# Optimization experiments

Hardware: AMD Instinct MI355X
Metric: run time of the kernel (lower is better)

The kernel has to match this reference:

```python
import jax, jax.numpy as jnp
import numpy as np
import math

D_MODEL, N_HEADS, D_K, D_V = 512, 2, 64, 64
C_CLIP = 10.0
MASK_FILL = -10.0

def setup_inputs() -> dict:
    key = jax.random.key(0)
    ks = jax.random.split(key, 12)
    B, Lq, Lk = 4, 2048, 2048
    s = 1.0 / math.sqrt(D_MODEL)
    return {
        "Q": jax.random.normal(ks[0], (B, Lq, D_MODEL), jnp.float32),
        "K": jax.random.normal(ks[1], (B, Lk, D_MODEL), jnp.float32),
        "V": jax.random.normal(ks[2], (B, Lk, D_MODEL), jnp.float32),
        "mask": jax.random.randint(ks[3], (B, Lk), 0, 2) > 0,
        "Wq": jax.random.normal(ks[4], (D_MODEL, N_HEADS * D_K), jnp.float32) * s,
        "bq": jnp.zeros((N_HEADS * D_K,), jnp.float32),
        "Wk": jax.random.normal(ks[5], (D_MODEL, N_HEADS * D_K), jnp.float32) * s,
        "bk": jnp.zeros((N_HEADS * D_K,), jnp.float32),
        "Wv": jax.random.normal(ks[6], (D_MODEL, N_HEADS * D_V), jnp.float32) * s,
        "bv": jnp.zeros((N_HEADS * D_V,), jnp.float32),
        "Wo": jax.random.normal(ks[7], (N_HEADS * D_V, D_MODEL), jnp.float32) * s,
        "bo": jnp.zeros((D_MODEL,), jnp.float32),
    }

def reference(Q, K, V, mask, Wq, bq, Wk, bk, Wv, bv, Wo, bo):
    B, Lq, _ = Q.shape
    Lk = K.shape[1]
    # project and split heads: [B, h, L, d]
    q = (Q @ Wq + bq).reshape(B, Lq, N_HEADS, D_K).transpose(0, 2, 1, 3)
    k = (K @ Wk + bk).reshape(B, Lk, N_HEADS, D_K).transpose(0, 2, 1, 3)
    v = (V @ Wv + bv).reshape(B, Lk, N_HEADS, D_V).transpose(0, 2, 1, 3)
    scores = jnp.einsum("bhqd,bhkd->bhqk", q, k) / jnp.sqrt(jnp.float32(D_K))
    scores = jnp.tanh(scores) * C_CLIP
    scores = jnp.where(mask[:, None, None, :], MASK_FILL, scores)
    attn = jax.nn.log_softmax(scores, axis=-1)  # NOTE: log-softmax used directly as weights
    out = jnp.einsum("bhqk,bhkd->bhqd", attn, v)
    out = out.transpose(0, 2, 1, 3).reshape(B, Lq, N_HEADS * D_V)
    out = out @ Wo + bo
    return (out, attn)
```

## Files before the change

kernel.cpp:

```cpp
#include <hip/hip_runtime.h>

typedef __attribute__((ext_vector_type(8))) short short8;
typedef __attribute__((ext_vector_type(4))) short short4v;
typedef __attribute__((ext_vector_type(4))) float f32x4;

#define DEVI static __device__ __forceinline__

constexpr int NB   = 4;
constexpr int NH   = 2;
constexpr int SEQ  = 2048;
constexpr int DM   = 512;
constexpr int DKV  = 64;
constexpr int HDIM = 128;

DEVI unsigned short f2bf(float f) {
    union { float f; unsigned u; } v; v.f = f;
    unsigned r = v.u + 0x7FFFu + ((v.u >> 16) & 1u);
    return (unsigned short)(r >> 16);
}
DEVI float bf2f(unsigned short s) {
    union { unsigned u; float f; } v; v.u = ((unsigned)s) << 16; return v.f;
}
DEVI void async16(const void* g, void* l) {
    __builtin_amdgcn_global_load_lds(
        (const __attribute__((address_space(1))) unsigned int*)g,
        (__attribute__((address_space(3))) unsigned int*)l, 16, 0, 0);
}

__global__ __launch_bounds__(256) void k_prep(
    const float* __restrict__ Wq, const float* __restrict__ Wk,
    const float* __restrict__ Wv, const float* __restrict__ Wo,
    unsigned short* __restrict__ Wqt, unsigned short* __restrict__ Wkt,
    unsigned short* __restrict__ Wvt, unsigned short* __restrict__ Wot) {
    int id = blockIdx.x * 256 + threadIdx.x;
    int which = id >> 16;
    int rem = id & 65535;
    if (which < 3) {
        const float* W = which == 0 ? Wq : (which == 1 ? Wk : Wv);
        unsigned short* Wt = which == 0 ? Wqt : (which == 1 ? Wkt : Wvt);
        int n = rem >> 9, k = rem & 511;
        Wt[rem] = f2bf(W[k * HDIM + n]);
    } else {
        int n = rem >> 7, k = rem & 127;
        Wot[rem] = f2bf(Wo[k * DM + n]);
    }
}

__global__ __launch_bounds__(256) void k_proj(
    const float* __restrict__ Qg, const float* __restrict__ Kg, const float* __restrict__ Vg,
    const unsigned short* __restrict__ Wqt, const unsigned short* __restrict__ Wkt,
    const unsigned short* __restrict__ Wvt,
    const float* __restrict__ bq, const float* __restrict__ bk, const float* __restrict__ bv,
    unsigned short* __restrict__ qs, unsigned short* __restrict__ kb,
    unsigned short* __restrict__ vt) {
    __shared__ unsigned short lA[64 * 64];
    __shared__ unsigned short lB[128 * 64];

    const int y = blockIdx.y;
    const float* X = y == 0 ? Qg : (y == 1 ? Kg : Vg);
    const unsigned short* Wt = y == 0 ? Wqt : (y == 1 ? Wkt : Wvt);
    const float* bias = y == 0 ? bq : (y == 1 ? bk : bv);
    const float scal = y == 0 ? 0.125f : 1.0f;
    const int row0 = blockIdx.x * 64;
    const int tid = threadIdx.x, lane = tid & 63, wv = tid >> 6;
    const int l16 = lane & 15, lq4 = lane >> 4;
    const int wr = wv >> 1, wc = wv & 1;

    f32x4 acc[2][4];
    #pragma unroll
    for (int i = 0; i < 2; ++i)
        #pragma unroll
        for (int j = 0; j < 4; ++j) acc[i][j] = f32x4{0.f, 0.f, 0.f, 0.f};

    const int arow = tid >> 2, ac0 = (tid & 3) * 16;

    for (int kc = 0; kc < 8; ++kc) {
        {
            const float* src = X + (size_t)(row0 + arow) * DM + kc * 64 + ac0;
            unsigned short* dst = &lA[arow * 64 + ac0];
            #pragma unroll
            for (int i = 0; i < 4; ++i) {
                float4 v = *(const float4*)(src + 4 * i);
                unsigned p0 = (unsigned)f2bf(v.x) | ((unsigned)f2bf(v.y) << 16);
                unsigned p1 = (unsigned)f2bf(v.z) | ((unsigned)f2bf(v.w) << 16);
                *(unsigned*)(dst + 4 * i) = p0;
                *(unsigned*)(dst + 4 * i + 2) = p1;
            }
        }
        #pragma unroll
        for (int c = 0; c < 4; ++c) {
            int chunk = wv * 4 + c;
            int n = chunk * 8 + (lane >> 3);
            int kpart = (lane & 7) * 8;
            const void* g = (const char*)Wt + ((size_t)n * DM + kc * 64 + kpart) * 2;
            void* l = (char*)lB + chunk * 1024 + lane * 16;
            async16(g, l);
        }
        __syncthreads();

        #pragma unroll
        for (int ks = 0; ks < 2; ++ks) {
            short8 a[2], b[4];
            #pragma unroll
            for (int mt = 0; mt < 2; ++mt) {
                int m = wr * 32 + mt * 16 + l16;
                a[mt] = *(const short8*)&lA[m * 64 + ks * 32 + lq4 * 8];
            }
            #pragma unroll
            for (int nt = 0; nt < 4; ++nt) {
                int n = wc * 64 + nt * 16 + l16;
                b[nt] = *(const short8*)&lB[n * 64 + ks * 32 + lq4 * 8];
            }
            #pragma unroll
            for (int mt = 0; mt < 2; ++mt)
                #pragma unroll
                for (int nt = 0; nt < 4; ++nt)
                    acc[mt][nt] = __builtin_amdgcn_mfma_f32_16x16x32_bf16(
                        a[mt], b[nt], acc[mt][nt], 0, 0, 0);
        }
        __syncthreads();
    }

    if (y < 2) {
        unsigned short* dstp = (y == 0) ? qs : kb;
        #pragma unroll
        for (int mt = 0; mt < 2; ++mt)
            #pragma unroll
            for (int nt = 0; nt < 4; ++nt) {
                int col = wc * 64 + nt * 16 + l16;
                float bb = bias[col];
                int h = col >> 6, d = col & 63;
                #pragma unroll
                for (int r = 0; r < 4; ++r) {
                    int row = row0 + wr * 32 + mt * 16 + lq4 * 4 + r;
                    int b = row >> 11, pos = row & 2047;
                    float val = (acc[mt][nt][r] + bb) * scal;
                    dstp[((size_t)(b * NH + h) * SEQ + pos) * DKV + d] = f2bf(val);
                }
            }
    } else {
        #pragma unroll
        for (int mt = 0; mt < 2; ++mt)
            #pragma unroll
            for (int nt = 0; nt < 4; ++nt) {
                int col = wc * 64 + nt * 16 + l16;
                float bb = bias[col];
                #pragma unroll
                for (int r = 0; r < 4; ++r) {
                    int mrow = wr * 32 + mt * 16 + lq4 * 4 + r;
                    lB[col * 64 + mrow] = f2bf(acc[mt][nt][r] + bb);
                }
            }
        __syncthreads();
        int c = tid >> 1, mp = (tid & 1) * 32;
        int b = row0 >> 11, kpos0 = row0 & 2047;
        int h = c >> 6, d = c & 63;
        unsigned short* dst = vt + ((size_t)(b * NH + h) * DKV + d) * SEQ + kpos0 + mp;
        const unsigned short* srcl = &lB[c * 64 + mp];
        #pragma unroll
        for (int i = 0; i < 4; ++i)
            *(uint4*)(dst + 8 * i) = *(const uint4*)(srcl + 8 * i);
    }
}

__global__ __launch_bounds__(256) void k_pass1(
    const unsigned short* __restrict__ qs, const unsigned short* __restrict__ kb,
    const int* __restrict__ maskg, float* __restrict__ Lpart) {
    __shared__ unsigned short lK[128 * 64];
    __shared__ int lM[128];
    __shared__ float lsumW[4 * 64];

    const int bx = blockIdx.x;
    const int ksp = bx & 3;
    const int qt = (bx >> 2) & 31;
    const int bh = bx >> 7;
    const int qbase = qt * 64;
    const int b = bh >> 1;
    const int tid = threadIdx.x, lane = tid & 63, wv = tid >> 6;
    const int l16 = lane & 15, lq4 = lane >> 4;

    short8 aq[4][2];
    #pragma unroll
    for (int mt = 0; mt < 4; ++mt)
        #pragma unroll
        for (int ks = 0; ks < 2; ++ks) {
            size_t off = ((size_t)bh * SEQ + qbase + mt * 16 + l16) * DKV + ks * 32 + lq4 * 8;
            aq[mt][ks] = *(const short8*)(qs + off);
        }

    float sums[4][4];
    #pragma unroll
    for (int mt = 0; mt < 4; ++mt)
        #pragma unroll
        for (int r = 0; r < 4; ++r) sums[mt][r] = 0.f;

    const char* kbase_ptr = (const char*)(kb + (size_t)bh * SEQ * DKV);

    for (int kt = ksp * 4; kt < ksp * 4 + 4; ++kt) {
        int kbase = kt * 128;
        #pragma unroll
        for (int c = 0; c < 4; ++c) {
            int chunk = wv * 4 + c;
            const void* g = kbase_ptr + (size_t)kbase * 128 + chunk * 1024 + lane * 16;
            void* l = (char*)lK + chunk * 1024 + lane * 16;
            async16(g, l);
        }
        if (tid < 128) lM[tid] = maskg[b * SEQ + kbase + tid];
        __syncthreads();

        f32x4 acc[4][2];
        #pragma unroll
        for (int mt = 0; mt < 4; ++mt)
            #pragma unroll
            for (int nt = 0; nt < 2; ++nt) acc[mt][nt] = f32x4{0.f, 0.f, 0.f, 0.f};
        #pragma unroll
        for (int ks = 0; ks < 2; ++ks) {
            short8 bfr[2];
            #pragma unroll
            for (int nt = 0; nt < 2; ++nt) {
                int n = wv * 32 + nt * 16 + l16;
                bfr[nt] = *(const short8*)&lK[n * 64 + ks * 32 + lq4 * 8];
            }
            #pragma unroll
            for (int mt = 0; mt < 4; ++mt)
                #pragma unroll
                for (int nt = 0; nt < 2; ++nt)
                    acc[mt][nt] = __builtin_amdgcn_mfma_f32_16x16x32_bf16(
                        aq[mt][ks], bfr[nt], acc[mt][nt], 0, 0, 0);
        }
        #pragma unroll
        for (int nt = 0; nt < 2; ++nt) {
            int col = wv * 32 + nt * 16 + l16;
            int mv = lM[col];
            #pragma unroll
            for (int mt = 0; mt < 4; ++mt)
                #pragma unroll
                for (int r = 0; r < 4; ++r) {
                    float x = acc[mt][nt][r];
                    float e2 = __expf(2.f * x);
                    float s10 = 10.f - 20.f * __builtin_amdgcn_rcpf(1.f + e2);
                    float s = mv ? -10.f : s10;
                    sums[mt][r] += __expf(s);
                }
        }
        __syncthreads();
    }

    #pragma unroll
    for (int mt = 0; mt < 4; ++mt)
        #pragma unroll
        for (int r = 0; r < 4; ++r) {
            float v = sums[mt][r];
            v += __shfl_xor(v, 1); v += __shfl_xor(v, 2);
            v += __shfl_xor(v, 4); v += __shfl_xor(v, 8);
            if (l16 == 0) lsumW[wv * 64 + mt * 16 + lq4 * 4 + r] = v;
        }
    __syncthreads();
    if (tid < 64) {
        float v = lsumW[tid] + lsumW[64 + tid] + lsumW[128 + tid] + lsumW[192 + tid];
        Lpart[(size_t)ksp * (8 * SEQ) + (size_t)bh * SEQ + qbase + tid] = v;
    }
}

__global__ __launch_bounds__(256) void k_pass2(
    const unsigned short* __restrict__ qs, const unsigned short* __restrict__ kb,
    const unsigned short* __restrict__ vt, const int* __restrict__ maskg,
    const float* __restrict__ Lpart, float* __restrict__ attnG, float* __restrict__ outh2) {
    __shared__ unsigned short lK[128 * 64];
    __shared__ unsigned short lV[64 * 128];
    __shared__ unsigned short lAttn[64 * 136];
    __shared__ int lM[128];

    const int bx = blockIdx.x;
    const int ksp = bx & 3;
    const int qt = (bx >> 2) & 31;
    const int bh = bx >> 7;
    const int qbase = qt * 64;
    const int b = bh >> 1, h = bh & 1;
    const int tid = threadIdx.x, lane = tid & 63, wv = tid >> 6;
    const int l16 = lane & 15, lq4 = lane >> 4;

    short8 aq[4][2];
    #pragma unroll
    for (int mt = 0; mt < 4; ++mt)
        #pragma unroll
        for (int ks = 0; ks < 2; ++ks) {
            size_t off = ((size_t)bh * SEQ + qbase + mt * 16 + l16) * DKV + ks * 32 + lq4 * 8;
            aq[mt][ks] = *(const short8*)(qs + off);
        }

    float Lr[4][4];
    #pragma unroll
    for (int mt = 0; mt < 4; ++mt)
        #pragma unroll
        for (int r = 0; r < 4; ++r) {
            size_t idx = (size_t)bh * SEQ + qbase + mt * 16 + lq4 * 4 + r;
            float s = Lpart[idx] + Lpart[8 * SEQ + idx] +
                      Lpart[2 * 8 * SEQ + idx] + Lpart[3 * 8 * SEQ + idx];
            Lr[mt][r] = __logf(s);
        }

    f32x4 o[4];
    #pragma unroll
    for (int mt = 0; mt < 4; ++mt) o[mt] = f32x4{0.f, 0.f, 0.f, 0.f};

    const char* kbase_ptr = (const char*)(kb + (size_t)bh * SEQ * DKV);

    for (int kt = ksp * 4; kt < ksp * 4 + 4; ++kt) {
        int kbase = kt * 128;
        #pragma unroll
        for (int c = 0; c < 4; ++c) {
            int chunk = wv * 4 + c;
            const void* g = kbase_ptr + (size_t)kbase * 128 + chunk * 1024 + lane * 16;
            void* l = (char*)lK + chunk * 1024 + lane * 16;
            async16(g, l);
        }
        #pragma unroll
        for (int c = 0; c < 4; ++c) {
            int chunk = wv * 4 + c;
            int d = chunk * 4 + (lane >> 4);
            int kk = (lane & 15) * 8;
            const void* g = (const char*)vt + (((size_t)bh * DKV + d) * SEQ + kbase + kk) * 2;
            void* l = (char*)lV + chunk * 1024 + lane * 16;
            async16(g, l);
        }
        if (tid < 128) lM[tid] = maskg[b * SEQ + kbase + tid];
        __syncthreads();

        f32x4 s[4][2];
        #pragma unroll
        for (int mt = 0; mt < 4; ++mt)
            #pragma unroll
            for (int nt = 0; nt < 2; ++nt) s[mt][nt] = f32x4{0.f, 0.f, 0.f, 0.f};
        #pragma unroll
        for (int ks = 0; ks < 2; ++ks) {
            short8 bfr[2];
            #pragma unroll
            for (int nt = 0; nt < 2; ++nt) {
                int n = wv * 32 + nt * 16 + l16;
                bfr[nt] = *(const short8*)&lK[n * 64 + ks * 32 + lq4 * 8];
            }
            #pragma unroll
            for (int mt = 0; mt < 4; ++mt)
                #pragma unroll
                for (int nt = 0; nt < 2; ++nt)
                    s[mt][nt] = __builtin_amdgcn_mfma_f32_16x16x32_bf16(
                        aq[mt][ks], bfr[nt], s[mt][nt], 0, 0, 0);
        }
        #pragma unroll
        for (int nt = 0; nt < 2; ++nt) {
            int col = wv * 32 + nt * 16 + l16;
            int mv = lM[col];
            #pragma unroll
            for (int mt = 0; mt < 4; ++mt)
                #pragma unroll
                for (int r = 0; r < 4; ++r) {
                    float x = s[mt][nt][r];
                    float e2 = __expf(2.f * x);
                    float s10 = 10.f - 20.f * __builtin_amdgcn_rcpf(1.f + e2);
                    float a = (mv ? -10.f : s10) - Lr[mt][r];
                    lAttn[(mt * 16 + lq4 * 4 + r) * 136 + col] = f2bf(a);
                }
        }
        __syncthreads();

        #pragma unroll
        for (int ks = 0; ks < 4; ++ks) {
            short8 bfr = *(const short8*)&lV[(wv * 16 + l16) * 128 + ks * 32 + lq4 * 8];
            #pragma unroll
            for (int mt = 0; mt < 4; ++mt) {
                short8 af = *(const short8*)&lAttn[(mt * 16 + l16) * 136 + ks * 32 + lq4 * 8];
                o[mt] = __builtin_amdgcn_mfma_f32_16x16x32_bf16(af, bfr, o[mt], 0, 0, 0);
            }
        }
        #pragma unroll
        for (int j = 0; j < 8; ++j) {
            int row = j * 8 + (tid >> 5);
            int col = (tid & 31) * 4;
            short4v hv = *(const short4v*)&lAttn[row * 136 + col];
            float4 f;
            f.x = bf2f((unsigned short)hv[0]); f.y = bf2f((unsigned short)hv[1]);
            f.z = bf2f((unsigned short)hv[2]); f.w = bf2f((unsigned short)hv[3]);
            float* gdst = attnG + ((size_t)bh * SEQ + qbase + row) * SEQ + kbase + col;
            *(float4*)gdst = f;
        }
        __syncthreads();
    }

    float* dst = outh2 + (size_t)ksp * (8192 * HDIM);
    #pragma unroll
    for (int mt = 0; mt < 4; ++mt)
        #pragma unroll
        for (int r = 0; r < 4; ++r) {
            int q = qbase + mt * 16 + lq4 * 4 + r;
            int dcol = wv * 16 + l16;
            dst[((size_t)b * SEQ + q) * HDIM + h * DKV + dcol] = o[mt][r];
        }
}

__global__ __launch_bounds__(256) void k_comb(const float* __restrict__ outh2,
                                              unsigned short* __restrict__ outh) {
    int i = (blockIdx.x * 256 + threadIdx.x) * 4;
    float4 a = *(const float4*)(outh2 + i);
    float4 c = *(const float4*)(outh2 + 1048576 + i);
    float4 d = *(const float4*)(outh2 + 2 * 1048576 + i);
    float4 e = *(const float4*)(outh2 + 3 * 1048576 + i);
    unsigned long long pk =
        (unsigned long long)f2bf(a.x + c.x + d.x + e.x) |
        ((unsigned long long)f2bf(a.y + c.y + d.y + e.y) << 16) |
        ((unsigned long long)f2bf(a.z + c.z + d.z + e.z) << 32) |
        ((unsigned long long)f2bf(a.w + c.w + d.w + e.w) << 48);
    *(unsigned long long*)(outh + i) = pk;
}

__global__ __launch_bounds__(256) void k_oproj(
    const unsigned short* __restrict__ outh, const unsigned short* __restrict__ Wot,
    const float* __restrict__ bo, float* __restrict__ outG) {
    __shared__ unsigned short lA2[128 * 128];
    __shared__ unsigned short lB2[128 * 128];
    const int row0 = blockIdx.x * 128, col0 = blockIdx.y * 128;
    const int tid = threadIdx.x, lane = tid & 63, wv = tid >> 6;
    const int l16 = lane & 15, lq4 = lane >> 4;
    const int wr = wv >> 1, wc = wv & 1;

    #pragma unroll
    for (int c = 0; c < 8; ++c) {
        int chunk = wv * 8 + c;
        const void* g = (const char*)outh + (size_t)row0 * 256 + chunk * 1024 + lane * 16;
        void* l = (char*)lA2 + chunk * 1024 + lane * 16;
        async16(g, l);
    }
    #pragma unroll
    for (int c = 0; c < 8; ++c) {
        int chunk = wv * 8 + c;
        const void* g = (const char*)Wot + (size_t)col0 * 256 + chunk * 1024 + lane * 16;
        void* l = (char*)lB2 + chunk * 1024 + lane * 16;
        async16(g, l);
    }
    __syncthreads();

    f32x4 acc[4][4];
    #pragma unroll
    for (int mt = 0; mt < 4; ++mt)
        #pragma unroll
        for (int nt = 0; nt < 4; ++nt) acc[mt][nt] = f32x4{0.f, 0.f, 0.f, 0.f};

    #pragma unroll
    for (int ks = 0; ks < 4; ++ks) {
        short8 a[4], bfr[4];
        #pragma unroll
        for (int mt = 0; mt < 4; ++mt)
            a[mt] = *(const short8*)&lA2[(wr * 64 + mt * 16 + l16) * 128 + ks * 32 + lq4 * 8];
        #pragma unroll
        for (int nt = 0; nt < 4; ++nt)
            bfr[nt] = *(const short8*)&lB2[(wc * 64 + nt * 16 + l16) * 128 + ks * 32 + lq4 * 8];
        #pragma unroll
        for (int mt = 0; mt < 4; ++mt)
            #pragma unroll
            for (int nt = 0; nt < 4; ++nt)
                acc[mt][nt] = __builtin_amdgcn_mfma_f32_16x16x32_bf16(
                    a[mt], bfr[nt], acc[mt][nt], 0, 0, 0);
    }

    #pragma unroll
    for (int nt = 0; nt < 4; ++nt) {
        int col = col0 + wc * 64 + nt * 16 + l16;
        float bb = bo[col];
        #pragma unroll
        for (int mt = 0; mt < 4; ++mt)
            #pragma unroll
            for (int r = 0; r < 4; ++r) {
                int row = row0 + wr * 64 + mt * 16 + lq4 * 4 + r;
                outG[(size_t)row * DM + col] = acc[mt][nt][r] + bb;
            }
    }
}

extern "C" void kernel_launch(void* const* d_in, const int* in_sizes, int n_in,
                              void* d_out, int out_size, void* d_ws, size_t ws_size,
                              hipStream_t stream) {
    (void)in_sizes; (void)n_in; (void)out_size; (void)ws_size;
    const float* Qg = (const float*)d_in[0];
    const float* Kg = (const float*)d_in[1];
    const float* Vg = (const float*)d_in[2];
    const int*   maskg = (const int*)d_in[3];
    const float* Wq = (const float*)d_in[4];
    const float* bq = (const float*)d_in[5];
    const float* Wk = (const float*)d_in[6];
    const float* bk = (const float*)d_in[7];
    const float* Wv = (const float*)d_in[8];
    const float* bv = (const float*)d_in[9];
    const float* Wo = (const float*)d_in[10];
    const float* bo = (const float*)d_in[11];

    char* ws = (char*)d_ws;
    unsigned short* qs   = (unsigned short*)(ws);
    unsigned short* kb   = (unsigned short*)(ws + (4  << 20));
    unsigned short* vt   = (unsigned short*)(ws + (8  << 20));
    float*          outh2= (float*)(ws + (12 << 20));
    unsigned short* outh = (unsigned short*)(ws + (28 << 20));
    float*          Lpart= (float*)(ws + (30 << 20));
    unsigned short* Wqt  = (unsigned short*)(ws + (30 << 20) + 262144);
    unsigned short* Wkt  = (unsigned short*)((char*)Wqt + 131072);
    unsigned short* Wvt  = (unsigned short*)((char*)Wkt + 131072);
    unsigned short* Wot  = (unsigned short*)((char*)Wvt + 131072);

    float* outG  = (float*)d_out;
    float* attnG = outG + (size_t)NB * SEQ * DM;

    hipLaunchKernelGGL(k_prep, dim3(1024), dim3(256), 0, stream,
                       Wq, Wk, Wv, Wo, Wqt, Wkt, Wvt, Wot);
    hipLaunchKernelGGL(k_proj, dim3(128, 3), dim3(256), 0, stream,
                       Qg, Kg, Vg, Wqt, Wkt, Wvt, bq, bk, bv, qs, kb, vt);
    hipLaunchKernelGGL(k_pass1, dim3(1024), dim3(256), 0, stream, qs, kb, maskg, Lpart);
    hipLaunchKernelGGL(k_pass2, dim3(1024), dim3(256), 0, stream,
                       qs, kb, vt, maskg, Lpart, attnG, outh2);
    hipLaunchKernelGGL(k_comb, dim3(1024), dim3(256), 0, stream, outh2, outh);
    hipLaunchKernelGGL(k_oproj, dim3(64, 4), dim3(256), 0, stream, outh, Wot, bo, outG);
}
```

Before: 262.9 us.

## Fuse attention passes into one kernel holding full score rows in LDS

Replaces the two-pass attention (sum pass, recompute-and-write pass) and the split-K combine kernel with one kernel. Each 512-thread block holds a 32-query by 2048-key bf16 score tile in 128KB of LDS, computes the log-sum-exp from it, writes the fp32 attention weights, then runs the PV matmul straight from LDS. This removes the recomputation of QK^T, the partial-sum buffers and the extra launch. It also adds XOR swizzling to the LDS tiles in the projection and output-projection kernels to reduce bank conflicts. The tradeoffs are one block per CU from the large LDS footprint and K/V fragments read straight from global memory without staging.

Result: slower. 281.8 us (+7.2%).

```diff
diff --git a/kernel.cpp b/kernel.cpp
--- a/kernel.cpp
+++ b/kernel.cpp
@@ -1,7 +1,6 @@
 #include <hip/hip_runtime.h>
 
 typedef __attribute__((ext_vector_type(8))) short short8;
-typedef __attribute__((ext_vector_type(4))) short short4v;
 typedef __attribute__((ext_vector_type(4))) float f32x4;
 
 #define DEVI static __device__ __forceinline__
@@ -77,22 +76,23 @@
     for (int kc = 0; kc < 8; ++kc) {
         {
             const float* src = X + (size_t)(row0 + arow) * DM + kc * 64 + ac0;
-            unsigned short* dst = &lA[arow * 64 + ac0];
             #pragma unroll
             for (int i = 0; i < 4; ++i) {
                 float4 v = *(const float4*)(src + 4 * i);
                 unsigned p0 = (unsigned)f2bf(v.x) | ((unsigned)f2bf(v.y) << 16);
                 unsigned p1 = (unsigned)f2bf(v.z) | ((unsigned)f2bf(v.w) << 16);
-                *(unsigned*)(dst + 4 * i) = p0;
-                *(unsigned*)(dst + 4 * i + 2) = p1;
+                int slot = ((tid & 3) * 2 + (i >> 1)) ^ (arow & 7);
+                char* d = (char*)lA + arow * 128 + slot * 16 + (i & 1) * 8;
+                *(unsigned*)d = p0;
+                *(unsigned*)(d + 4) = p1;
             }
         }
         #pragma unroll
         for (int c = 0; c < 4; ++c) {
             int chunk = wv * 4 + c;
             int n = chunk * 8 + (lane >> 3);
-            int kpart = (lane & 7) * 8;
-            const void* g = (const char*)Wt + ((size_t)n * DM + kc * 64 + kpart) * 2;
+            int gslot = (lane & 7) ^ (n & 7);
+            const void* g = (const char*)Wt + ((size_t)n * DM + kc * 64) * 2 + gslot * 16;
             void* l = (char*)lB + chunk * 1024 + lane * 16;
             async16(g, l);
         }
@@ -104,12 +104,14 @@
             #pragma unroll
             for (int mt = 0; mt < 2; ++mt) {
                 int m = wr * 32 + mt * 16 + l16;
-                a[mt] = *(const short8*)&lA[m * 64 + ks * 32 + lq4 * 8];
+                unsigned ao = (unsigned)(m * 128 + ks * 64 + lq4 * 16) ^ ((unsigned)(m & 7) << 4);
+                a[mt] = *(const short8*)((const char*)lA + ao);
             }
             #pragma unroll
             for (int nt = 0; nt < 4; ++nt) {
                 int n = wc * 64 + nt * 16 + l16;
-                b[nt] = *(const short8*)&lB[n * 64 + ks * 32 + lq4 * 8];
+                unsigned bo2 = (unsigned)(n * 128 + ks * 64 + lq4 * 16) ^ ((unsigned)(n & 7) << 4);
+                b[nt] = *(const short8*)((const char*)lB + bo2);
             }
             #pragma unroll
             for (int mt = 0; mt < 2; ++mt)
@@ -163,254 +165,119 @@
     }
 }
 
-__global__ __launch_bounds__(256) void k_pass1(
-    const unsigned short* __restrict__ qs, const unsigned short* __restrict__ kb,
-    const int* __restrict__ maskg, float* __restrict__ Lpart) {
-    __shared__ unsigned short lK[128 * 64];
-    __shared__ int lM[128];
-    __shared__ float lsumW[4 * 64];
-
-    const int bx = blockIdx.x;
-    const int ksp = bx & 3;
-    const int qt = (bx >> 2) & 31;
-    const int bh = bx >> 7;
-    const int qbase = qt * 64;
-    const int b = bh >> 1;
-    const int tid = threadIdx.x, lane = tid & 63, wv = tid >> 6;
-    const int l16 = lane & 15, lq4 = lane >> 4;
-
-    short8 aq[4][2];
-    #pragma unroll
-    for (int mt = 0; mt < 4; ++mt)
-        #pragma unroll
-        for (int ks = 0; ks < 2; ++ks) {
-            size_t off = ((size_t)bh * SEQ + qbase + mt * 16 + l16) * DKV + ks * 32 + lq4 * 8;
-            aq[mt][ks] = *(const short8*)(qs + off);
-        }
-
-    float sums[4][4];
-    #pragma unroll
-    for (int mt = 0; mt < 4; ++mt)
-        #pragma unroll
-        for (int r = 0; r < 4; ++r) sums[mt][r] = 0.f;
-
-    const char* kbase_ptr = (const char*)(kb + (size_t)bh * SEQ * DKV);
-
-    for (int kt = ksp * 4; kt < ksp * 4 + 4; ++kt) {
-        int kbase = kt * 128;
-        #pragma unroll
-        for (int c = 0; c < 4; ++c) {
-            int chunk = wv * 4 + c;
-            const void* g = kbase_ptr + (size_t)kbase * 128 + chunk * 1024 + lane * 16;
-            void* l = (char*)lK + chunk * 1024 + lane * 16;
-            async16(g, l);
-        }
-        if (tid < 128) lM[tid] = maskg[b * SEQ + kbase + tid];
-        __syncthreads();
-
-        f32x4 acc[4][2];
-        #pragma unroll
-        for (int mt = 0; mt < 4; ++mt)
-            #pragma unroll
-            for (int nt = 0; nt < 2; ++nt) acc[mt][nt] = f32x4{0.f, 0.f, 0.f, 0.f};
-        #pragma unroll
-        for (int ks = 0; ks < 2; ++ks) {
-            short8 bfr[2];
-            #pragma unroll
-            for (int nt = 0; nt < 2; ++nt) {
-                int n = wv * 32 + nt * 16 + l16;
-                bfr[nt] = *(const short8*)&lK[n * 64 + ks * 32 + lq4 * 8];
-            }
-            #pragma unroll
-            for (int mt = 0; mt < 4; ++mt)
-                #pragma unroll
-                for (int nt = 0; nt < 2; ++nt)
-                    acc[mt][nt] = __builtin_amdgcn_mfma_f32_16x16x32_bf16(
-                        aq[mt][ks], bfr[nt], acc[mt][nt], 0, 0, 0);
-        }
-        #pragma unroll
-        for (int nt = 0; nt < 2; ++nt) {
-            int col = wv * 32 + nt * 16 + l16;
-            int mv = lM[col];
-            #pragma unroll
-            for (int mt = 0; mt < 4; ++mt)
-                #pragma unroll
-                for (int r = 0; r < 4; ++r) {
-                    float x = acc[mt][nt][r];
-                    float e2 = __expf(2.f * x);
-                    float s10 = 10.f - 20.f * __builtin_amdgcn_rcpf(1.f + e2);
-                    float s = mv ? -10.f : s10;
-                    sums[mt][r] += __expf(s);
-                }
-        }
-        __syncthreads();
-    }
-
-    #pragma unroll
-    for (int mt = 0; mt < 4; ++mt)
-        #pragma unroll
-        for (int r = 0; r < 4; ++r) {
-            float v = sums[mt][r];
-            v += __shfl_xor(v, 1); v += __shfl_xor(v, 2);
-            v += __shfl_xor(v, 4); v += __shfl_xor(v, 8);
-            if (l16 == 0) lsumW[wv * 64 + mt * 16 + lq4 * 4 + r] = v;
-        }
-    __syncthreads();
-    if (tid < 64) {
-        float v = lsumW[tid] + lsumW[64 + tid] + lsumW[128 + tid] + lsumW[192 + tid];
-        Lpart[(size_t)ksp * (8 * SEQ) + (size_t)bh * SEQ + qbase + tid] = v;
-    }
-}
-
-__global__ __launch_bounds__(256) void k_pass2(
+__global__ __launch_bounds__(512) void k_fused(
     const unsigned short* __restrict__ qs, const unsigned short* __restrict__ kb,
     const unsigned short* __restrict__ vt, const int* __restrict__ maskg,
-    const float* __restrict__ Lpart, float* __restrict__ attnG, float* __restrict__ outh2) {
-    __shared__ unsigned short lK[128 * 64];
-    __shared__ unsigned short lV[64 * 128];
-    __shared__ unsigned short lAttn[64 * 136];
-    __shared__ int lM[128];
-
-    const int bx = blockIdx.x;
-    const int ksp = bx & 3;
-    const int qt = (bx >> 2) & 31;
-    const int bh = bx >> 7;
-    const int qbase = qt * 64;
+    float* __restrict__ attnG, unsigned short* __restrict__ outh) {
+    __shared__ unsigned short sAttn[32 * 2048];
+    __shared__ float lsum[4][32];
+    __shared__ float lL[32];
+
+    const int wg = blockIdx.x;
+    const int swz = (wg & 7) * 64 + (wg >> 3);
+    const int bh = swz >> 6;
+    const int qt = swz & 63;
+    const int qbase = qt * 32;
     const int b = bh >> 1, h = bh & 1;
     const int tid = threadIdx.x, lane = tid & 63, wv = tid >> 6;
     const int l16 = lane & 15, lq4 = lane >> 4;
-
-    short8 aq[4][2];
-    #pragma unroll
-    for (int mt = 0; mt < 4; ++mt)
-        #pragma unroll
-        for (int ks = 0; ks < 2; ++ks) {
-            size_t off = ((size_t)bh * SEQ + qbase + mt * 16 + l16) * DKV + ks * 32 + lq4 * 8;
-            aq[mt][ks] = *(const short8*)(qs + off);
-        }
-
-    float Lr[4][4];
-    #pragma unroll
-    for (int mt = 0; mt < 4; ++mt)
+    const int wr = wv >> 2, wc = wv & 3;
+
+    const unsigned short* qrow =
+        qs + ((size_t)bh * SEQ + qbase + wr * 16 + l16) * DKV + lq4 * 8;
+    short8 aq0 = *(const short8*)qrow;
+    short8 aq1 = *(const short8*)(qrow + 32);
+
+    const unsigned short* kfrag =
+        kb + ((size_t)bh * SEQ + wc * 16 + l16) * DKV + lq4 * 8;
+    const int* mrow = maskg + b * SEQ + wc * 16 + l16;
+
+    const int srow_q = wr * 16 + lq4 * 4;
+    const int cbase = wc * 16 + l16;
+
+    float sums[4] = {0.f, 0.f, 0.f, 0.f};
+
+    #pragma unroll 2
+    for (int kt = 0; kt < 32; ++kt) {
+        short8 b0 = *(const short8*)(kfrag + (size_t)kt * 4096);
+        short8 b1 = *(const short8*)(kfrag + (size_t)kt * 4096 + 32);
+        int mv = mrow[kt * 64];
+        f32x4 acc = f32x4{0.f, 0.f, 0.f, 0.f};
+        acc = __builtin_amdgcn_mfma_f32_16x16x32_bf16(aq0, b0, acc, 0, 0, 0);
+        acc = __builtin_amdgcn_mfma_f32_16x16x32_bf16(aq1, b1, acc, 0, 0, 0);
+        int col = kt * 64 + cbase;
         #pragma unroll
         for (int r = 0; r < 4; ++r) {
-            size_t idx = (size_t)bh * SEQ + qbase + mt * 16 + lq4 * 4 + r;
-            float s = Lpart[idx] + Lpart[8 * SEQ + idx] +
-                      Lpart[2 * 8 * SEQ + idx] + Lpart[3 * 8 * SEQ + idx];
-            Lr[mt][r] = __logf(s);
-        }
-
-    f32x4 o[4];
-    #pragma unroll
-    for (int mt = 0; mt < 4; ++mt) o[mt] = f32x4{0.f, 0.f, 0.f, 0.f};
-
-    const char* kbase_ptr = (const char*)(kb + (size_t)bh * SEQ * DKV);
-
-    for (int kt = ksp * 4; kt < ksp * 4 + 4; ++kt) {
-        int kbase = kt * 128;
-        #pragma unroll
-        for (int c = 0; c < 4; ++c) {
-            int chunk = wv * 4 + c;
-            const void* g = kbase_ptr + (size_t)kbase * 128 + chunk * 1024 + lane * 16;
-            void* l = (char*)lK + chunk * 1024 + lane * 16;
-            async16(g, l);
-        }
-        #pragma unroll
-        for (int c = 0; c < 4; ++c) {
-            int chunk = wv * 4 + c;
-            int d = chunk * 4 + (lane >> 4);
-            int kk = (lane & 15) * 8;
-            const void* g = (const char*)vt + (((size_t)bh * DKV + d) * SEQ + kbase + kk) * 2;
-            void* l = (char*)lV + chunk * 1024 + lane * 16;
-            async16(g, l);
-        }
-        if (tid < 128) lM[tid] = maskg[b * SEQ + kbase + tid];
-        __syncthreads();
-
-        f32x4 s[4][2];
-        #pragma unroll
-        for (int mt = 0; mt < 4; ++mt)
-            #pragma unroll
-            for (int nt = 0; nt < 2; ++nt) s[mt][nt] = f32x4{0.f, 0.f, 0.f, 0.f};
-        #pragma unroll
-        for (int ks = 0; ks < 2; ++ks) {
-            short8 bfr[2];
-            #pragma unroll
-            for (int nt = 0; nt < 2; ++nt) {
-                int n = wv * 32 + nt * 16 + l16;
-                bfr[nt] = *(const short8*)&lK[n * 64 + ks * 32 + lq4 * 8];
-            }
-            #pragma unroll
-            for (int mt = 0; mt < 4; ++mt)
-                #pragma unroll
-                for (int nt = 0; nt < 2; ++nt)
-                    s[mt][nt] = __builtin_amdgcn_mfma_f32_16x16x32_bf16(
-                        aq[mt][ks], bfr[nt], s[mt][nt], 0, 0, 0);
-        }
-        #pragma unroll
-        for (int nt = 0; nt < 2; ++nt) {
-            int col = wv * 32 + nt * 16 + l16;
-            int mv = lM[col];
-            #pragma unroll
-            for (int mt = 0; mt < 4; ++mt)
-                #pragma unroll
-                for (int r = 0; r < 4; ++r) {
-                    float x = s[mt][nt][r];
-                    float e2 = __expf(2.f * x);
-                    float s10 = 10.f - 20.f * __builtin_amdgcn_rcpf(1.f + e2);
-                    float a = (mv ? -10.f : s10) - Lr[mt][r];
-                    lAttn[(mt * 16 + lq4 * 4 + r) * 136 + col] = f2bf(a);
-                }
-        }
-        __syncthreads();
-
-        #pragma unroll
-        for (int ks = 0; ks < 4; ++ks) {
-            short8 bfr = *(const short8*)&lV[(wv * 16 + l16) * 128 + ks * 32 + lq4 * 8];
-            #pragma unroll
-            for (int mt = 0; mt < 4; ++mt) {
-                short8 af = *(const short8*)&lAttn[(mt * 16 + l16) * 136 + ks * 32 + lq4 * 8];
-                o[mt] = __builtin_amdgcn_mfma_f32_16x16x32_bf16(af, bfr, o[mt], 0, 0, 0);
-            }
-        }
-        #pragma unroll
-        for (int j = 0; j < 8; ++j) {
-            int row = j * 8 + (tid >> 5);
-            int col = (tid & 31) * 4;
-            short4v hv = *(const short4v*)&lAttn[row * 136 + col];
-            float4 f;
-            f.x = bf2f((unsigned short)hv[0]); f.y = bf2f((unsigned short)hv[1]);
-            f.z = bf2f((unsigned short)hv[2]); f.w = bf2f((unsigned short)hv[3]);
-            float* gdst = attnG + ((size_t)bh * SEQ + qbase + row) * SEQ + kbase + col;
-            *(float4*)gdst = f;
-        }
-        __syncthreads();
-    }
-
-    float* dst = outh2 + (size_t)ksp * (8192 * HDIM);
-    #pragma unroll
-    for (int mt = 0; mt < 4; ++mt)
-        #pragma unroll
-        for (int r = 0; r < 4; ++r) {
-            int q = qbase + mt * 16 + lq4 * 4 + r;
-            int dcol = wv * 16 + l16;
-            dst[((size_t)b * SEQ + q) * HDIM + h * DKV + dcol] = o[mt][r];
-        }
-}
-
-__global__ __launch_bounds__(256) void k_comb(const float* __restrict__ outh2,
-                                              unsigned short* __restrict__ outh) {
-    int i = (blockIdx.x * 256 + threadIdx.x) * 4;
-    float4 a = *(const float4*)(outh2 + i);
-    float4 c = *(const float4*)(outh2 + 1048576 + i);
-    float4 d = *(const float4*)(outh2 + 2 * 1048576 + i);
-    float4 e = *(const float4*)(outh2 + 3 * 1048576 + i);
-    unsigned long long pk =
-        (unsigned long long)f2bf(a.x + c.x + d.x + e.x) |
-        ((unsigned long long)f2bf(a.y + c.y + d.y + e.y) << 16) |
-        ((unsigned long long)f2bf(a.z + c.z + d.z + e.z) << 32) |
-        ((unsigned long long)f2bf(a.w + c.w + d.w + e.w) << 48);
-    *(unsigned long long*)(outh + i) = pk;
+            float x = acc[r];
+            float e2 = __expf(2.f * x);
+            float s10 = 10.f - 20.f * __builtin_amdgcn_rcpf(1.f + e2);
+            float s = mv ? -10.f : s10;
+            sums[r] += __expf(s);
+            int row = srow_q + r;
+            unsigned bo = (unsigned)(row * 4096 + col * 2) ^ ((unsigned)(row & 7) << 4);
+            *(unsigned short*)((char*)sAttn + bo) = f2bf(s);
+        }
+    }
+
+    #pragma unroll
+    for (int r = 0; r < 4; ++r) {
+        float v = sums[r];
+        v += __shfl_xor(v, 1); v += __shfl_xor(v, 2);
+        v += __shfl_xor(v, 4); v += __shfl_xor(v, 8);
+        if (l16 == 0) lsum[wc][srow_q + r] = v;
+    }
+    __syncthreads();
+    if (tid < 32)
+        lL[tid] = __logf(lsum[0][tid] + lsum[1][tid] + lsum[2][tid] + lsum[3][tid]);
+    __syncthreads();
+
+    {
+        const int row = tid >> 4;
+        const int cb = (tid & 15) * 8;
+        const float Lv = lL[row];
+        float* gdst = attnG + ((size_t)bh * SEQ + qbase + row) * SEQ;
+        const unsigned rbase = (unsigned)(row * 4096);
+        const unsigned rxor = (unsigned)(row & 7) << 4;
+        #pragma unroll
+        for (int j = 0; j < 16; ++j) {
+            int c = cb + j * 128;
+            unsigned bo = (rbase + (unsigned)(c * 2)) ^ rxor;
+            short8 v = *(const short8*)((const char*)sAttn + bo);
+            float fv[8];
+            #pragma unroll
+            for (int t = 0; t < 8; ++t) fv[t] = bf2f((unsigned short)v[t]) - Lv;
+            float4 fa, fb;
+            fa.x = fv[0]; fa.y = fv[1]; fa.z = fv[2]; fa.w = fv[3];
+            fb.x = fv[4]; fb.y = fv[5]; fb.z = fv[6]; fb.w = fv[7];
+            *(float4*)(gdst + c) = fa;
+            *(float4*)(gdst + c + 4) = fb;
+            short8 w;
+            #pragma unroll
+            for (int t = 0; t < 8; ++t) w[t] = (short)f2bf(fv[t]);
+            *(short8*)((char*)sAttn + bo) = w;
+        }
+    }
+    __syncthreads();
+
+    const unsigned short* vfrag =
+        vt + ((size_t)bh * DKV + wc * 16 + l16) * SEQ + lq4 * 8;
+    const int arow = wr * 16 + l16;
+    const unsigned abase = (unsigned)(arow * 4096);
+    const unsigned axor = (unsigned)(arow & 7) << 4;
+    f32x4 o = f32x4{0.f, 0.f, 0.f, 0.f};
+    #pragma unroll 4
+    for (int ks = 0; ks < 64; ++ks) {
+        short8 af = *(const short8*)((const char*)sAttn +
+                                     ((abase + (unsigned)(ks * 64 + lq4 * 16)) ^ axor));
+        short8 vf = *(const short8*)(vfrag + ks * 32);
+        o = __builtin_amdgcn_mfma_f32_16x16x32_bf16(af, vf, o, 0, 0, 0);
+    }
+
+    #pragma unroll
+    for (int r = 0; r < 4; ++r) {
+        size_t orow = (size_t)b * SEQ + qbase + wr * 16 + lq4 * 4 + r;
+        outh[orow * HDIM + h * DKV + wc * 16 + l16] = f2bf(o[r]);
+    }
 }
 
 __global__ __launch_bounds__(256) void k_oproj(
@@ -426,16 +293,18 @@
     #pragma unroll
     for (int c = 0; c < 8; ++c) {
         int chunk = wv * 8 + c;
-        const void* g = (const char*)outh + (size_t)row0 * 256 + chunk * 1024 + lane * 16;
-        void* l = (char*)lA2 + chunk * 1024 + lane * 16;
-        async16(g, l);
+        int row = chunk * 4 + (lane >> 4);
+        int gslot = (lane & 15) ^ (row & 7);
+        async16((const char*)outh + ((size_t)(row0 + row)) * 256 + gslot * 16,
+                (char*)lA2 + chunk * 1024 + lane * 16);
     }
     #pragma unroll
     for (int c = 0; c < 8; ++c) {
         int chunk = wv * 8 + c;
-        const void* g = (const char*)Wot + (size_t)col0 * 256 + chunk * 1024 + lane * 16;
-        void* l = (char*)lB2 + chunk * 1024 + lane * 16;
-        async16(g, l);
+        int row = chunk * 4 + (lane >> 4);
+        int gslot = (lane & 15) ^ (row & 7);
+        async16((const char*)Wot + ((size_t)(col0 + row)) * 256 + gslot * 16,
+                (char*)lB2 + chunk * 1024 + lane * 16);
     }
     __syncthreads();
 
@@ -449,11 +318,17 @@
     for (int ks = 0; ks < 4; ++ks) {
         short8 a[4], bfr[4];
         #pragma unroll
-        for (int mt = 0; mt < 4; ++mt)
-            a[mt] = *(const short8*)&lA2[(wr * 64 + mt * 16 + l16) * 128 + ks * 32 + lq4 * 8];
-        #pragma unroll
-        for (int nt = 0; nt < 4; ++nt)
-            bfr[nt] = *(const short8*)&lB2[(wc * 64 + nt * 16 + l16) * 128 + ks * 32 + lq4 * 8];
+        for (int mt = 0; mt < 4; ++mt) {
+            int m = wr * 64 + mt * 16 + l16;
+            unsigned ao = (unsigned)(m * 256 + ks * 64 + lq4 * 16) ^ ((unsigned)(m & 7) << 4);
+            a[mt] = *(const short8*)((const char*)lA2 + ao);
+        }
+        #pragma unroll
+        for (int nt = 0; nt < 4; ++nt) {
+            int n = wc * 64 + nt * 16 + l16;
+            unsigned bo2 = (unsigned)(n * 256 + ks * 64 + lq4 * 16) ^ ((unsigned)(n & 7) << 4);
+            bfr[nt] = *(const short8*)((const char*)lB2 + bo2);
+        }
         #pragma unroll
         for (int mt = 0; mt < 4; ++mt)
             #pragma unroll
@@ -497,9 +372,7 @@
     unsigned short* qs   = (unsigned short*)(ws);
     unsigned short* kb   = (unsigned short*)(ws + (4  << 20));
     unsigned short* vt   = (unsigned short*)(ws + (8  << 20));
-    float*          outh2= (float*)(ws + (12 << 20));
     unsigned short* outh = (unsigned short*)(ws + (28 << 20));
-    float*          Lpart= (float*)(ws + (30 << 20));
     unsigned short* Wqt  = (unsigned short*)(ws + (30 << 20) + 262144);
     unsigned short* Wkt  = (unsigned short*)((char*)Wqt + 131072);
     unsigned short* Wvt  = (unsigned short*)((char*)Wkt + 131072);
@@ -512,9 +385,7 @@
                        Wq, Wk, Wv, Wo, Wqt, Wkt, Wvt, Wot);
     hipLaunchKernelGGL(k_proj, dim3(128, 3), dim3(256), 0, stream,
                        Qg, Kg, Vg, Wqt, Wkt, Wvt, bq, bk, bv, qs, kb, vt);
-    hipLaunchKernelGGL(k_pass1, dim3(1024), dim3(256), 0, stream, qs, kb, maskg, Lpart);
-    hipLaunchKernelGGL(k_pass2, dim3(1024), dim3(256), 0, stream,
-                       qs, kb, vt, maskg, Lpart, attnG, outh2);
-    hipLaunchKernelGGL(k_comb, dim3(1024), dim3(256), 0, stream, outh2, outh);
+    hipLaunchKernelGGL(k_fused, dim3(512), dim3(512), 0, stream,
+                       qs, kb, vt, maskg, attnG, outh);
     hipLaunchKernelGGL(k_oproj, dim3(64, 4), dim3(256), 0, stream, outh, Wot, bo, outG);
 }
```

## Fuse split-K combine into output projection, tile weight transpose, swizzle LDS

Applied to the files above, without the earlier changes.

Removes the separate k_comb kernel. The output-projection kernel now reads the four fp32 split partials directly, sums them, converts to bf16 and writes them into LDS. The weight-prep kernel now does a tiled transpose through shared memory with vectorized loads and stores, replacing strided scalar accesses. An XOR swizzle is applied to LDS rows in k_oproj to cut bank conflicts. The trade-off is that each of the 4 column blocks of k_oproj re-reads and re-sums the same partials, so fp32 partial traffic is multiplied by four.

New measurement: 259.3 us. About the same (-1.4%).

```diff
diff --git a/kernel.cpp b/kernel.cpp
--- a/kernel.cpp
+++ b/kernel.cpp
@@ -21,6 +21,9 @@
 DEVI float bf2f(unsigned short s) {
     union { unsigned u; float f; } v; v.u = ((unsigned)s) << 16; return v.f;
 }
+DEVI unsigned pk2(float a, float b) {
+    return (unsigned)f2bf(a) | ((unsigned)f2bf(b) << 16);
+}
 DEVI void async16(const void* g, void* l) {
     __builtin_amdgcn_global_load_lds(
         (const __attribute__((address_space(1))) unsigned int*)g,
@@ -32,18 +35,37 @@
     const float* __restrict__ Wv, const float* __restrict__ Wo,
     unsigned short* __restrict__ Wqt, unsigned short* __restrict__ Wkt,
     unsigned short* __restrict__ Wvt, unsigned short* __restrict__ Wot) {
-    int id = blockIdx.x * 256 + threadIdx.x;
-    int which = id >> 16;
-    int rem = id & 65535;
-    if (which < 3) {
-        const float* W = which == 0 ? Wq : (which == 1 ? Wk : Wv);
-        unsigned short* Wt = which == 0 ? Wqt : (which == 1 ? Wkt : Wvt);
-        int n = rem >> 9, k = rem & 511;
-        Wt[rem] = f2bf(W[k * HDIM + n]);
+    __shared__ unsigned short T[64][72];
+    const int bid = blockIdx.x, tid = threadIdx.x;
+    const float* src; unsigned short* dst; int ss, ds, k0, n0;
+    if (bid < 48) {
+        int m = bid >> 4, t16 = bid & 15;
+        src = m == 0 ? Wq : (m == 1 ? Wk : Wv);
+        dst = m == 0 ? Wqt : (m == 1 ? Wkt : Wvt);
+        ss = 128; ds = 512;
+        k0 = (t16 >> 1) * 64; n0 = (t16 & 1) * 64;
     } else {
-        int n = rem >> 7, k = rem & 127;
-        Wot[rem] = f2bf(Wo[k * DM + n]);
-    }
+        int t16 = bid - 48;
+        src = Wo; dst = Wot; ss = 512; ds = 128;
+        k0 = (t16 >> 3) * 64; n0 = (t16 & 7) * 64;
+    }
+    const int kk = tid >> 4, nn4 = (tid & 15) * 4;
+    #pragma unroll
+    for (int i = 0; i < 4; ++i) {
+        float4 v = *(const float4*)(src + (size_t)(k0 + kk + i * 16) * ss + n0 + nn4);
+        T[kk + i * 16][nn4]     = f2bf(v.x);
+        T[kk + i * 16][nn4 + 1] = f2bf(v.y);
+        T[kk + i * 16][nn4 + 2] = f2bf(v.z);
+        T[kk + i * 16][nn4 + 3] = f2bf(v.w);
+    }
+    __syncthreads();
+    const int nn = tid >> 2, kc = (tid & 3) * 16;
+    unsigned short tmp[16];
+    #pragma unroll
+    for (int i = 0; i < 16; ++i) tmp[i] = T[kc + i][nn];
+    unsigned short* o = dst + (size_t)(n0 + nn) * ds + k0 + kc;
+    *(uint4*)o       = *(uint4*)tmp;
+    *(uint4*)(o + 8) = *(uint4*)(tmp + 8);
 }
 
 __global__ __launch_bounds__(256) void k_proj(
@@ -398,23 +420,8 @@
         }
 }
 
-__global__ __launch_bounds__(256) void k_comb(const float* __restrict__ outh2,
-                                              unsigned short* __restrict__ outh) {
-    int i = (blockIdx.x * 256 + threadIdx.x) * 4;
-    float4 a = *(const float4*)(outh2 + i);
-    float4 c = *(const float4*)(outh2 + 1048576 + i);
-    float4 d = *(const float4*)(outh2 + 2 * 1048576 + i);
-    float4 e = *(const float4*)(outh2 + 3 * 1048576 + i);
-    unsigned long long pk =
-        (unsigned long long)f2bf(a.x + c.x + d.x + e.x) |
-        ((unsigned long long)f2bf(a.y + c.y + d.y + e.y) << 16) |
-        ((unsigned long long)f2bf(a.z + c.z + d.z + e.z) << 32) |
-        ((unsigned long long)f2bf(a.w + c.w + d.w + e.w) << 48);
-    *(unsigned long long*)(outh + i) = pk;
-}
-
 __global__ __launch_bounds__(256) void k_oproj(
-    const unsigned short* __restrict__ outh, const unsigned short* __restrict__ Wot,
+    const float* __restrict__ outh2, const unsigned short* __restrict__ Wot,
     const float* __restrict__ bo, float* __restrict__ outG) {
     __shared__ unsigned short lA2[128 * 128];
     __shared__ unsigned short lB2[128 * 128];
@@ -426,16 +433,29 @@
     #pragma unroll
     for (int c = 0; c < 8; ++c) {
         int chunk = wv * 8 + c;
-        const void* g = (const char*)outh + (size_t)row0 * 256 + chunk * 1024 + lane * 16;
-        void* l = (char*)lA2 + chunk * 1024 + lane * 16;
-        async16(g, l);
-    }
-    #pragma unroll
-    for (int c = 0; c < 8; ++c) {
-        int chunk = wv * 8 + c;
-        const void* g = (const char*)Wot + (size_t)col0 * 256 + chunk * 1024 + lane * 16;
-        void* l = (char*)lB2 + chunk * 1024 + lane * 16;
-        async16(g, l);
+        int row = chunk * 4 + (lane >> 4);
+        int gslot = (lane & 15) ^ (row & 7);
+        async16((const char*)Wot + ((size_t)(col0 + row)) * 256 + gslot * 16,
+                (char*)lB2 + chunk * 1024 + lane * 16);
+    }
+    {
+        const int c16 = tid & 31;
+        const int rb = tid >> 5;
+        #pragma unroll
+        for (int i = 0; i < 16; ++i) {
+            int r = rb + i * 8;
+            size_t off = (size_t)(row0 + r) * 128 + c16 * 4;
+            float4 a = *(const float4*)(outh2 + off);
+            float4 b = *(const float4*)(outh2 + 1048576 + off);
+            float4 c = *(const float4*)(outh2 + 2 * 1048576 + off);
+            float4 d = *(const float4*)(outh2 + 3 * 1048576 + off);
+            unsigned p0 = pk2(a.x + b.x + c.x + d.x, a.y + b.y + c.y + d.y);
+            unsigned p1 = pk2(a.z + b.z + c.z + d.z, a.w + b.w + c.w + d.w);
+            unsigned long long pk =
+                (unsigned long long)p0 | ((unsigned long long)p1 << 32);
+            unsigned bo2 = (unsigned)(r * 256 + c16 * 8) ^ ((unsigned)(r & 7) << 4);
+            *(unsigned long long*)((char*)lA2 + bo2) = pk;
+        }
     }
     __syncthreads();
 
@@ -449,11 +469,17 @@
     for (int ks = 0; ks < 4; ++ks) {
         short8 a[4], bfr[4];
         #pragma unroll
-        for (int mt = 0; mt < 4; ++mt)
-            a[mt] = *(const short8*)&lA2[(wr * 64 + mt * 16 + l16) * 128 + ks * 32 + lq4 * 8];
-        #pragma unroll
-        for (int nt = 0; nt < 4; ++nt)
-            bfr[nt] = *(const short8*)&lB2[(wc * 64 + nt * 16 + l16) * 128 + ks * 32 + lq4 * 8];
+        for (int mt = 0; mt < 4; ++mt) {
+            int m = wr * 64 + mt * 16 + l16;
+            unsigned ao = (unsigned)(m * 256 + ks * 64 + lq4 * 16) ^ ((unsigned)(m & 7) << 4);
+            a[mt] = *(const short8*)((const char*)lA2 + ao);
+        }
+        #pragma unroll
+        for (int nt = 0; nt < 4; ++nt) {
+            int n = wc * 64 + nt * 16 + l16;
+            unsigned bo2 = (unsigned)(n * 256 + ks * 64 + lq4 * 16) ^ ((unsigned)(n & 7) << 4);
+            bfr[nt] = *(const short8*)((const char*)lB2 + bo2);
+        }
         #pragma unroll
         for (int mt = 0; mt < 4; ++mt)
             #pragma unroll
@@ -498,7 +524,6 @@
     unsigned short* kb   = (unsigned short*)(ws + (4  << 20));
     unsigned short* vt   = (unsigned short*)(ws + (8  << 20));
     float*          outh2= (float*)(ws + (12 << 20));
-    unsigned short* outh = (unsigned short*)(ws + (28 << 20));
     float*          Lpart= (float*)(ws + (30 << 20));
     unsigned short* Wqt  = (unsigned short*)(ws + (30 << 20) + 262144);
     unsigned short* Wkt  = (unsigned short*)((char*)Wqt + 131072);
@@ -508,13 +533,12 @@
     float* outG  = (float*)d_out;
     float* attnG = outG + (size_t)NB * SEQ * DM;
 
-    hipLaunchKernelGGL(k_prep, dim3(1024), dim3(256), 0, stream,
+    hipLaunchKernelGGL(k_prep, dim3(64), dim3(256), 0, stream,
                        Wq, Wk, Wv, Wo, Wqt, Wkt, Wvt, Wot);
     hipLaunchKernelGGL(k_proj, dim3(128, 3), dim3(256), 0, stream,
                        Qg, Kg, Vg, Wqt, Wkt, Wvt, bq, bk, bv, qs, kb, vt);
     hipLaunchKernelGGL(k_pass1, dim3(1024), dim3(256), 0, stream, qs, kb, maskg, Lpart);
     hipLaunchKernelGGL(k_pass2, dim3(1024), dim3(256), 0, stream,
                        qs, kb, vt, maskg, Lpart, attnG, outh2);
-    hipLaunchKernelGGL(k_comb, dim3(1024), dim3(256), 0, stream, outh2, outh);
-    hipLaunchKernelGGL(k_oproj, dim3(64, 4), dim3(256), 0, stream, outh, Wot, bo, outG);
-}
+    hipLaunchKernelGGL(k_oproj, dim3(64, 4), dim3(256), 0, stream, outh2, Wot, bo, outG);
+}
```
